# Optimization experiments

Measured on AMD Instinct MI355X. Metric: run time of the kernel, lower is better.

## Reference

```python
import jax, jax.numpy as jnp
import numpy as np

B, N, NC, C = 8, 16384, 64, 256

def setup_inputs() -> dict:
    key = jax.random.key(0)
    k1, k2, k3, k4, k5, k6 = jax.random.split(key, 6)
    s = 1.0 / np.sqrt(C)
    return {
        "point_features": jax.random.normal(k1, (B, N, C), dtype=jnp.float32),
        "centroid_features": jax.random.normal(k2, (B, NC, C), dtype=jnp.float32),
        "W_p": jax.random.uniform(k3, (C, C), jnp.float32, -s, s),   # point_transform weight (in,out)
        "b_p": jax.random.uniform(k4, (C,), jnp.float32, -s, s),
        "W_c": jax.random.uniform(k5, (C, C), jnp.float32, -s, s),   # centroid_transform weight (in,out)
        "b_c": jax.random.uniform(k6, (C,), jnp.float32, -s, s),
    }

def reference(point_features, centroid_features, W_p, b_p, W_c, b_c):
    # Linear projections
    p_proj = jnp.einsum('bnc,cd->bnd', point_features, W_p) + b_p      # (B,N,C)
    c_proj = jnp.einsum('bkc,cd->bkd', centroid_features, W_c) + b_c   # (B,NC,C)
    # Unscaled cross-attention scores and softmax over centroids
    scores = jnp.einsum('bnd,bkd->bnk', p_proj, c_proj)                # (B,N,NC)
    weights = jax.nn.softmax(scores, axis=-1)
    # Weighted sum of RAW centroid features (values not projected)
    weighted = jnp.einsum('bnk,bkc->bnc', weights, centroid_features)  # (B,N,C)
    return point_features + weighted
```

## Files before the change

### kernel.cpp

```cpp
#include <hip/hip_runtime.h>

#define B_  8
#define N_  16384
#define NC_ 64
#define C_  256

typedef __attribute__((ext_vector_type(8))) short bf16x8;
typedef __attribute__((ext_vector_type(4))) float f32x4;

#define WS_GT   0
#define WS_BLOB 262144
#define WS_S0   786432
#define WS_WFB  788480
#define WS_H    789504
#define WS_BB   790528

__device__ __forceinline__ unsigned rne_bf16(float f) {
    unsigned u = __float_as_uint(f);
    return (u + 0x7fffu + ((u >> 16) & 1u)) >> 16;
}

__device__ __forceinline__ f32x4 mfma16(bf16x8 a, bf16x8 b, f32x4 c) {
    return __builtin_amdgcn_mfma_f32_16x16x32_bf16(a, b, c, 0, 0, 0);
}

__global__ __launch_bounds__(256) void k_p1(const float* __restrict__ Wp,
        const float* __restrict__ Wc, const float* __restrict__ bc,
        const float* __restrict__ bp, float* __restrict__ ws) {
    __shared__ float WpL[256];
    __shared__ float bpL[256];
    __shared__ float red[4];
    int c = blockIdx.x, t = threadIdx.x;
    WpL[t] = Wp[(size_t)c*C_ + t];
    bpL[t] = bp[t];
    float bcv = bc[t];
    __syncthreads();

    const float* wcr = Wc + (size_t)t*C_;
    float acc = 0.f;
    #pragma unroll 8
    for (int d = 0; d < C_; d += 4) {
        f32x4 wv = *(const f32x4*)(wcr + d);
        f32x4 wp = *(const f32x4*)(WpL + d);
        acc += wv[0]*wp[0] + wv[1]*wp[1] + wv[2]*wp[2] + wv[3]*wp[3];
    }
    ws[WS_GT/4 + c*C_ + t] = acc;

    float hp = bcv * WpL[t];
    #pragma unroll
    for (int m = 32; m; m >>= 1) hp += __shfl_xor(hp, m);
    if ((t & 63) == 0) red[t >> 6] = hp;
    __syncthreads();
    if (t == 0) ws[WS_H/4 + c] = red[0] + red[1] + red[2] + red[3];

    if (c == 0) {
        float aw = 0.f;
        #pragma unroll 8
        for (int d = 0; d < C_; d += 4) {
            f32x4 wv = *(const f32x4*)(wcr + d);
            f32x4 b4 = *(const f32x4*)(bpL + d);
            aw += wv[0]*b4[0] + wv[1]*b4[1] + wv[2]*b4[2] + wv[3]*b4[3];
        }
        ws[WS_WFB/4 + t] = aw;
        float pb = bcv * bpL[t];
        #pragma unroll
        for (int m = 32; m; m >>= 1) pb += __shfl_xor(pb, m);
        __syncthreads();
        if ((t & 63) == 0) red[t >> 6] = pb;
        __syncthreads();
        if (t == 0) ws[WS_BB/4] = red[0] + red[1] + red[2] + red[3];
    }
}

__global__ __launch_bounds__(256) void k_p2(const float* __restrict__ Cf,
        float* __restrict__ ws) {
    __shared__ float CfL[8][256];
    __shared__ float wfbL[256];
    int b = blockIdx.x >> 3, kg = blockIdx.x & 7;
    int t = threadIdx.x;
    const float* cfb = Cf + ((size_t)b*NC_ + kg*8)*C_;
    #pragma unroll
    for (int kk = 0; kk < 8; ++kk) CfL[kk][t] = cfb[kk*C_ + t];
    wfbL[t] = ws[WS_WFB/4 + t];
    float hv = ws[WS_H/4 + t];
    float bb = ws[WS_BB/4];
    __syncthreads();

    char* vhiB = (char*)ws + WS_BLOB + (size_t)b*65536;
    char* cftB = vhiB + 32768;

    #pragma unroll
    for (int kk = 0; kk < 8; ++kk) {
        unsigned offc = ((unsigned)(t*128 + (kg*8 + kk)*2)) ^ ((unsigned)(t & 7) << 4);
        *(unsigned short*)(cftB + offc) = (unsigned short)rne_bf16(CfL[kk][t]);
    }

    float acc[8];
    #pragma unroll
    for (int kk = 0; kk < 8; ++kk) acc[kk] = hv;
    const float* gtr = ws + WS_GT/4 + (size_t)t*C_;
    #pragma unroll 4
    for (int e = 0; e < C_; e += 4) {
        f32x4 g4 = *(const f32x4*)(gtr + e);
        #pragma unroll
        for (int kk = 0; kk < 8; ++kk) {
            f32x4 c4 = *(const f32x4*)(&CfL[kk][e]);
            acc[kk] += g4[0]*c4[0] + g4[1]*c4[1] + g4[2]*c4[2] + g4[3]*c4[3];
        }
    }
    #pragma unroll
    for (int kk = 0; kk < 8; ++kk) {
        int row = kg*8 + kk;
        unsigned off = ((unsigned)(row*512 + t*2)) ^ ((unsigned)(row & 15) << 4);
        *(unsigned short*)(vhiB + off) = (unsigned short)rne_bf16(acc[kk]);
    }

    int w = t >> 6, l = t & 63;
    #pragma unroll
    for (int kk = 2*w; kk < 2*w + 2; ++kk) {
        float s = 0.f;
        #pragma unroll
        for (int j = 0; j < 4; ++j) s += CfL[kk][l + 64*j] * wfbL[l + 64*j];
        #pragma unroll
        for (int m = 32; m; m >>= 1) s += __shfl_xor(s, m);
        if (l == 0) ws[WS_S0/4 + b*NC_ + kg*8 + kk] = s + bb;
    }
}

__global__ __launch_bounds__(512, 4) void k_main(const float* __restrict__ P,
        const char* __restrict__ blob, const float* __restrict__ s0g,
        float* __restrict__ out) {
    __shared__ __align__(16) char smem[81920];
    char* wbAll = smem + 65536;

    const int nb = N_ / 128;
    int b    = blockIdx.x / nb;
    int tile = blockIdx.x % nb;
    int row_blk = tile * 128;
    int tid = threadIdx.x;
    int w   = tid >> 6;
    int l   = tid & 63;
    int l15 = l & 15;
    int g   = l >> 4;

    int prow = row_blk + w*16 + l15;
    const float* Prow = P + ((size_t)b*N_ + prow)*C_ + g*8;
    f32x4 pf[16];
    #pragma unroll
    for (int kk = 0; kk < 8; ++kk) {
        pf[2*kk]   = *(const f32x4*)(Prow + kk*32);
        pf[2*kk+1] = *(const f32x4*)(Prow + kk*32 + 4);
    }
    f32x4 sacc[4];
    #pragma unroll
    for (int mf = 0; mf < 4; ++mf)
        sacc[mf] = *(const f32x4*)(s0g + b*NC_ + mf*16 + g*4);

    {
        const f32x4* src = (const f32x4*)(blob + (size_t)b*65536);
        f32x4* dst = (f32x4*)smem;
        #pragma unroll
        for (int i = 0; i < 8; ++i) dst[tid + i*512] = src[tid + i*512];
    }
    __syncthreads();

    #pragma unroll
    for (int kk = 0; kk < 8; ++kk) {
        bf16x8 phi, plo;
        #pragma unroll
        for (int h = 0; h < 2; ++h) {
            #pragma unroll
            for (int j = 0; j < 4; ++j) {
                float f  = pf[2*kk + h][j];
                unsigned hb = rne_bf16(f);
                float hf = __uint_as_float(hb << 16);
                unsigned lb = rne_bf16(f - hf);
                phi[h*4 + j] = (short)hb;
                plo[h*4 + j] = (short)lb;
            }
        }
        #pragma unroll
        for (int mf = 0; mf < 4; ++mf) {
            unsigned off = ((unsigned)((mf*16 + l15)*512 + kk*64 + g*16)) ^ ((unsigned)l15 << 4);
            bf16x8 vh = *(const bf16x8*)(smem + off);
            sacc[mf] = mfma16(vh, phi, sacc[mf]);
            sacc[mf] = mfma16(vh, plo, sacc[mf]);
        }
    }

    float mx = -3.0e38f;
    #pragma unroll
    for (int mf = 0; mf < 4; ++mf)
        #pragma unroll
        for (int r = 0; r < 4; ++r) mx = fmaxf(mx, sacc[mf][r]);
    mx = fmaxf(mx, __shfl_xor(mx, 16));
    mx = fmaxf(mx, __shfl_xor(mx, 32));
    float sum = 0.f;
    float pv[4][4];
    #pragma unroll
    for (int mf = 0; mf < 4; ++mf)
        #pragma unroll
        for (int r = 0; r < 4; ++r) {
            float e = __expf(sacc[mf][r] - mx);
            pv[mf][r] = e; sum += e;
        }
    sum += __shfl_xor(sum, 16);
    sum += __shfl_xor(sum, 32);
    float inv = 1.0f / sum;

    char* wb = wbAll + w*2048;
    #pragma unroll
    for (int mf = 0; mf < 4; ++mf) {
        unsigned w01 = rne_bf16(pv[mf][0]*inv) | (rne_bf16(pv[mf][1]*inv) << 16);
        unsigned w23 = rne_bf16(pv[mf][2]*inv) | (rne_bf16(pv[mf][3]*inv) << 16);
        unsigned off = ((unsigned)(l15*128 + mf*32 + g*8)) ^ ((unsigned)(l15 & 7) << 4);
        uint2 v; v.x = w01; v.y = w23;
        *(uint2*)(wb + off) = v;
    }

    f32x4 zero = {0.f, 0.f, 0.f, 0.f};
    f32x4 oacc[16];
    #pragma unroll
    for (int nf = 0; nf < 16; ++nf) oacc[nf] = zero;
    #pragma unroll
    for (int kk2 = 0; kk2 < 2; ++kk2) {
        unsigned woff = ((unsigned)(l15*128 + kk2*64 + g*16)) ^ ((unsigned)(l15 & 7) << 4);
        bf16x8 wf = *(const bf16x8*)(wb + woff);
        #pragma unroll
        for (int nf = 0; nf < 16; ++nf) {
            unsigned coff = ((unsigned)((nf*16 + l15)*128 + kk2*64 + g*16)) ^ ((unsigned)(l15 & 7) << 4);
            bf16x8 cf = *(const bf16x8*)(smem + 32768 + coff);
            oacc[nf] = mfma16(cf, wf, oacc[nf]);
        }
    }

    size_t rowbase = ((size_t)b*N_ + row_blk + w*16 + l15) * C_;
    #pragma unroll
    for (int nf = 0; nf < 16; ++nf) {
        size_t idx = rowbase + nf*16 + g*4;
        f32x4 pr = *(const f32x4*)(P + idx);
        f32x4 o  = oacc[nf];
        f32x4 res = {pr[0]+o[0], pr[1]+o[1], pr[2]+o[2], pr[3]+o[3]};
        *(f32x4*)(out + idx) = res;
    }
}

extern "C" void kernel_launch(void* const* d_in, const int* in_sizes, int n_in,
                              void* d_out, int out_size, void* d_ws, size_t ws_size,
                              hipStream_t stream) {
    const float* P  = (const float*)d_in[0];
    const float* Cf = (const float*)d_in[1];
    const float* Wp = (const float*)d_in[2];
    const float* bp = (const float*)d_in[3];
    const float* Wc = (const float*)d_in[4];
    const float* bc = (const float*)d_in[5];
    float* out = (float*)d_out;
    float* ws  = (float*)d_ws;

    k_p1<<<256, 256, 0, stream>>>(Wp, Wc, bc, bp, ws);
    k_p2<<<64, 256, 0, stream>>>(Cf, ws);
    k_main<<<B_*(N_/128), 512, 0, stream>>>(P, (const char*)d_ws + WS_BLOB,
                                            ws + WS_S0/4, out);
}
```

Baseline: 290.2 us.

## Reuse split-bf16 point registers for residual and read V/Cf blobs from global

The main kernel no longer stages the per-batch V and Cf blobs into LDS. It reads them straight from global/L2, with 64-row tiles and 256-thread blocks. The residual add now rebuilds P from the hi+lo bf16 split already held in registers instead of reading P from global a second time, which removes about a third of the HBM traffic. The Cf blob layout in k_p2 is permuted to match the new output column order, and P loads are prefetched two k-steps ahead. The trade-off is that the residual is only about 16-bit-mantissa accurate, and there are more L2 reads of the shared blobs.

```diff
diff --git a/kernel.cpp b/kernel.cpp
--- a/kernel.cpp
+++ b/kernel.cpp
@@ -19,7 +19,9 @@
     unsigned u = __float_as_uint(f);
     return (u + 0x7fffu + ((u >> 16) & 1u)) >> 16;
 }
-
+__device__ __forceinline__ float bf2f(short s) {
+    return __uint_as_float(((unsigned)(unsigned short)s) << 16);
+}
 __device__ __forceinline__ f32x4 mfma16(bf16x8 a, bf16x8 b, f32x4 c) {
     return __builtin_amdgcn_mfma_f32_16x16x32_bf16(a, b, c, 0, 0, 0);
 }
@@ -86,13 +88,18 @@
     float bb = ws[WS_BB/4];
     __syncthreads();
 
-    char* vhiB = (char*)ws + WS_BLOB + (size_t)b*65536;
-    char* cftB = vhiB + 32768;
-
-    #pragma unroll
-    for (int kk = 0; kk < 8; ++kk) {
-        unsigned offc = ((unsigned)(t*128 + (kg*8 + kk)*2)) ^ ((unsigned)(t & 7) << 4);
-        *(unsigned short*)(cftB + offc) = (unsigned short)rne_bf16(CfL[kk][t]);
+    char* vtB  = (char*)ws + WS_BLOB + (size_t)b*65536;
+    char* cftB = vtB + 32768;
+
+    {
+        int nf  = ((t >> 5) << 1) | ((t >> 2) & 1);
+        int rho = ((t >> 3) & 3) * 4 + (t & 3);
+        unsigned base = (unsigned)(nf*2048 + rho*128);
+        #pragma unroll
+        for (int kk = 0; kk < 8; ++kk) {
+            *(unsigned short*)(cftB + base + (kg*8 + kk)*2) =
+                (unsigned short)rne_bf16(CfL[kk][t]);
+        }
     }
 
     float acc[8];
@@ -111,8 +118,7 @@
     #pragma unroll
     for (int kk = 0; kk < 8; ++kk) {
         int row = kg*8 + kk;
-        unsigned off = ((unsigned)(row*512 + t*2)) ^ ((unsigned)(row & 15) << 4);
-        *(unsigned short*)(vhiB + off) = (unsigned short)rne_bf16(acc[kk]);
+        *(unsigned short*)(vtB + row*512 + t*2) = (unsigned short)rne_bf16(acc[kk]);
     }
 
     int w = t >> 6, l = t & 63;
@@ -127,65 +133,68 @@
     }
 }
 
-__global__ __launch_bounds__(512, 4) void k_main(const float* __restrict__ P,
+__global__ __launch_bounds__(256, 4) void k_main(const float* __restrict__ P,
         const char* __restrict__ blob, const float* __restrict__ s0g,
         float* __restrict__ out) {
-    __shared__ __align__(16) char smem[81920];
-    char* wbAll = smem + 65536;
-
-    const int nb = N_ / 128;
-    int b    = blockIdx.x / nb;
-    int tile = blockIdx.x % nb;
-    int row_blk = tile * 128;
+    __shared__ __align__(16) char wbAll[8192];
+
+    int b    = blockIdx.x >> 8;
+    int tile = blockIdx.x & 255;
     int tid = threadIdx.x;
     int w   = tid >> 6;
     int l   = tid & 63;
     int l15 = l & 15;
     int g   = l >> 4;
 
-    int prow = row_blk + w*16 + l15;
-    const float* Prow = P + ((size_t)b*N_ + prow)*C_ + g*8;
-    f32x4 pf[16];
-    #pragma unroll
-    for (int kk = 0; kk < 8; ++kk) {
-        pf[2*kk]   = *(const f32x4*)(Prow + kk*32);
-        pf[2*kk+1] = *(const f32x4*)(Prow + kk*32 + 4);
-    }
+    const char* blobV = blob + (size_t)b*65536;
+    const char* blobC = blobV + 32768;
+
+    int prow = tile*64 + w*16 + l15;
+    const float* Prow = P + ((size_t)b*N_ + prow)*C_;
+
     f32x4 sacc[4];
     #pragma unroll
     for (int mf = 0; mf < 4; ++mf)
         sacc[mf] = *(const f32x4*)(s0g + b*NC_ + mf*16 + g*4);
 
-    {
-        const f32x4* src = (const f32x4*)(blob + (size_t)b*65536);
-        f32x4* dst = (f32x4*)smem;
-        #pragma unroll
-        for (int i = 0; i < 8; ++i) dst[tid + i*512] = src[tid + i*512];
-    }
-    __syncthreads();
+    bf16x8 phi[8], plo[8];
+    f32x4 pA0 = *(const f32x4*)(Prow + g*8);
+    f32x4 pA1 = *(const f32x4*)(Prow + g*8 + 4);
+    f32x4 pB0 = *(const f32x4*)(Prow + g*8 + 32);
+    f32x4 pB1 = *(const f32x4*)(Prow + g*8 + 36);
 
     #pragma unroll
     for (int kk = 0; kk < 8; ++kk) {
-        bf16x8 phi, plo;
+        bf16x8 vh0 = *(const bf16x8*)(blobV + (0*16 + l15)*512 + kk*64 + g*16);
+        bf16x8 vh1 = *(const bf16x8*)(blobV + (1*16 + l15)*512 + kk*64 + g*16);
+        bf16x8 vh2 = *(const bf16x8*)(blobV + (2*16 + l15)*512 + kk*64 + g*16);
+        bf16x8 vh3 = *(const bf16x8*)(blobV + (3*16 + l15)*512 + kk*64 + g*16);
         #pragma unroll
         for (int h = 0; h < 2; ++h) {
+            f32x4 src = h ? pA1 : pA0;
             #pragma unroll
             for (int j = 0; j < 4; ++j) {
-                float f  = pf[2*kk + h][j];
+                float f  = src[j];
                 unsigned hb = rne_bf16(f);
                 float hf = __uint_as_float(hb << 16);
                 unsigned lb = rne_bf16(f - hf);
-                phi[h*4 + j] = (short)hb;
-                plo[h*4 + j] = (short)lb;
+                phi[kk][h*4 + j] = (short)hb;
+                plo[kk][h*4 + j] = (short)lb;
             }
         }
-        #pragma unroll
-        for (int mf = 0; mf < 4; ++mf) {
-            unsigned off = ((unsigned)((mf*16 + l15)*512 + kk*64 + g*16)) ^ ((unsigned)l15 << 4);
-            bf16x8 vh = *(const bf16x8*)(smem + off);
-            sacc[mf] = mfma16(vh, phi, sacc[mf]);
-            sacc[mf] = mfma16(vh, plo, sacc[mf]);
-        }
+        pA0 = pB0; pA1 = pB1;
+        if (kk < 6) {
+            pB0 = *(const f32x4*)(Prow + g*8 + (kk+2)*32);
+            pB1 = *(const f32x4*)(Prow + g*8 + (kk+2)*32 + 4);
+        }
+        sacc[0] = mfma16(vh0, phi[kk], sacc[0]);
+        sacc[1] = mfma16(vh1, phi[kk], sacc[1]);
+        sacc[2] = mfma16(vh2, phi[kk], sacc[2]);
+        sacc[3] = mfma16(vh3, phi[kk], sacc[3]);
+        sacc[0] = mfma16(vh0, plo[kk], sacc[0]);
+        sacc[1] = mfma16(vh1, plo[kk], sacc[1]);
+        sacc[2] = mfma16(vh2, plo[kk], sacc[2]);
+        sacc[3] = mfma16(vh3, plo[kk], sacc[3]);
     }
 
     float mx = -3.0e38f;
@@ -196,13 +205,12 @@
     mx = fmaxf(mx, __shfl_xor(mx, 16));
     mx = fmaxf(mx, __shfl_xor(mx, 32));
     float sum = 0.f;
-    float pv[4][4];
     #pragma unroll
     for (int mf = 0; mf < 4; ++mf)
         #pragma unroll
         for (int r = 0; r < 4; ++r) {
             float e = __expf(sacc[mf][r] - mx);
-            pv[mf][r] = e; sum += e;
+            sacc[mf][r] = e; sum += e;
         }
     sum += __shfl_xor(sum, 16);
     sum += __shfl_xor(sum, 32);
@@ -211,37 +219,32 @@
     char* wb = wbAll + w*2048;
     #pragma unroll
     for (int mf = 0; mf < 4; ++mf) {
-        unsigned w01 = rne_bf16(pv[mf][0]*inv) | (rne_bf16(pv[mf][1]*inv) << 16);
-        unsigned w23 = rne_bf16(pv[mf][2]*inv) | (rne_bf16(pv[mf][3]*inv) << 16);
+        unsigned w01 = rne_bf16(sacc[mf][0]*inv) | (rne_bf16(sacc[mf][1]*inv) << 16);
+        unsigned w23 = rne_bf16(sacc[mf][2]*inv) | (rne_bf16(sacc[mf][3]*inv) << 16);
         unsigned off = ((unsigned)(l15*128 + mf*32 + g*8)) ^ ((unsigned)(l15 & 7) << 4);
         uint2 v; v.x = w01; v.y = w23;
         *(uint2*)(wb + off) = v;
     }
-
-    f32x4 zero = {0.f, 0.f, 0.f, 0.f};
-    f32x4 oacc[16];
-    #pragma unroll
-    for (int nf = 0; nf < 16; ++nf) oacc[nf] = zero;
-    #pragma unroll
-    for (int kk2 = 0; kk2 < 2; ++kk2) {
-        unsigned woff = ((unsigned)(l15*128 + kk2*64 + g*16)) ^ ((unsigned)(l15 & 7) << 4);
-        bf16x8 wf = *(const bf16x8*)(wb + woff);
-        #pragma unroll
-        for (int nf = 0; nf < 16; ++nf) {
-            unsigned coff = ((unsigned)((nf*16 + l15)*128 + kk2*64 + g*16)) ^ ((unsigned)(l15 & 7) << 4);
-            bf16x8 cf = *(const bf16x8*)(smem + 32768 + coff);
-            oacc[nf] = mfma16(cf, wf, oacc[nf]);
-        }
-    }
-
-    size_t rowbase = ((size_t)b*N_ + row_blk + w*16 + l15) * C_;
+    unsigned woff0 = ((unsigned)(l15*128 +  0 + g*16)) ^ ((unsigned)(l15 & 7) << 4);
+    unsigned woff1 = ((unsigned)(l15*128 + 64 + g*16)) ^ ((unsigned)(l15 & 7) << 4);
+    bf16x8 wf0 = *(const bf16x8*)(wb + woff0);
+    bf16x8 wf1 = *(const bf16x8*)(wb + woff1);
+
+    size_t rowbase = ((size_t)b*N_ + prow) * C_;
     #pragma unroll
     for (int nf = 0; nf < 16; ++nf) {
-        size_t idx = rowbase + nf*16 + g*4;
-        f32x4 pr = *(const f32x4*)(P + idx);
-        f32x4 o  = oacc[nf];
-        f32x4 res = {pr[0]+o[0], pr[1]+o[1], pr[2]+o[2], pr[3]+o[3]};
-        *(f32x4*)(out + idx) = res;
+        const char* cbase = blobC + nf*2048 + l15*128 + g*16;
+        bf16x8 cf0 = *(const bf16x8*)(cbase);
+        bf16x8 cf1 = *(const bf16x8*)(cbase + 64);
+        f32x4 o = {0.f, 0.f, 0.f, 0.f};
+        o = mfma16(cf0, wf0, o);
+        o = mfma16(cf1, wf1, o);
+        int kf = nf >> 1, e0 = (nf & 1) * 4;
+        f32x4 res;
+        #pragma unroll
+        for (int r = 0; r < 4; ++r)
+            res[r] = bf2f(phi[kf][e0 + r]) + bf2f(plo[kf][e0 + r]) + o[r];
+        *(f32x4*)(out + rowbase + (nf >> 1)*32 + (nf & 1)*4 + g*8) = res;
     }
 }
 
@@ -259,6 +262,6 @@
 
     k_p1<<<256, 256, 0, stream>>>(Wp, Wc, bc, bp, ws);
     k_p2<<<64, 256, 0, stream>>>(Cf, ws);
-    k_main<<<B_*(N_/128), 512, 0, stream>>>(P, (const char*)d_ws + WS_BLOB,
-                                            ws + WS_S0/4, out);
-}
+    k_main<<<B_*(N_/64), 256, 0, stream>>>(P, (const char*)d_ws + WS_BLOB,
+                                           ws + WS_S0/4, out);
+}
```

Result: slower. 354.7 us (+22.2%).
